# Kernel optimization log

Hardware: AMD Instinct MI355X
Metric: run time of the kernel (lower is better)

## Reference

```python
import jax, jax.numpy as jnp
import numpy as np

CUTOFF_UPPER = 4.5
EYE3 = jnp.eye(3, dtype=jnp.float32)


def tensor_norm(t):
    return (t ** 2).sum((-2, -1))


def decompose_tensor(X):
    # X: [N, C, 3, 3]
    tr_mean = jnp.trace(X, axis1=-2, axis2=-1) / 3.0
    I = tr_mean[..., None, None] * EYE3
    Xt = jnp.swapaxes(X, -2, -1)
    A = 0.5 * (X - Xt)
    S = 0.5 * (X + Xt) - I
    return I, A, S


def chan_linear(T, W, b):
    # torch: Linear applied over the channel axis after permute(0,2,3,1)
    # T: [N, C, 3, 3], W: [C, C], b: [C]
    return jnp.einsum('nkij,ck->ncij', T, W) + b[None, :, None, None]


def setup_inputs() -> dict:
    key = jax.random.key(0)
    ks = jax.random.split(key, 16)
    Np1, H, R, E = 20001, 128, 64, 200000
    X = jax.random.normal(ks[0], (Np1, H, 3, 3), dtype=jnp.float32)
    edge_index = jax.random.randint(ks[1], (2, E), 0, Np1)
    edge_weight = jax.random.uniform(ks[2], (E,), dtype=jnp.float32) * CUTOFF_UPPER
    edge_attr = jax.random.normal(ks[3], (E, R), dtype=jnp.float32)
    s = lambda fin: 1.0 / np.sqrt(fin)
    W1 = jax.random.uniform(ks[4], (3, H, H), minval=-s(H), maxval=s(H), dtype=jnp.float32)
    b1 = jax.random.uniform(ks[5], (3, H), minval=-s(H), maxval=s(H), dtype=jnp.float32)
    W2a = jax.random.uniform(ks[6], (H, R), minval=-s(R), maxval=s(R), dtype=jnp.float32)
    b2a = jax.random.uniform(ks[7], (H,), minval=-s(R), maxval=s(R), dtype=jnp.float32)
    W2b = jax.random.uniform(ks[8], (2 * H, H), minval=-s(H), maxval=s(H), dtype=jnp.float32)
    b2b = jax.random.uniform(ks[9], (2 * H,), minval=-s(H), maxval=s(H), dtype=jnp.float32)
    W2c = jax.random.uniform(ks[10], (3 * H, 2 * H), minval=-s(2 * H), maxval=s(2 * H), dtype=jnp.float32)
    b2c = jax.random.uniform(ks[11], (3 * H,), minval=-s(2 * H), maxval=s(2 * H), dtype=jnp.float32)
    W3 = jax.random.uniform(ks[12], (3, H, H), minval=-s(H), maxval=s(H), dtype=jnp.float32)
    b3 = jax.random.uniform(ks[13], (3, H), minval=-s(H), maxval=s(H), dtype=jnp.float32)
    return dict(X=X, edge_index=edge_index, edge_weight=edge_weight, edge_attr=edge_attr,
                W1=W1, b1=b1, W2a=W2a, b2a=b2a, W2b=W2b, b2b=b2b, W2c=W2c, b2c=b2c, W3=W3, b3=b3)


def reference(X, edge_index, edge_weight, edge_attr, W1, b1, W2a, b2a, W2b, b2b, W2c, b2c, W3, b3):
    Np1, H = X.shape[0], X.shape[1]
    act = jax.nn.silu
    X = X / (tensor_norm(X) + 1.0)[..., None, None]
    I, A, S = decompose_tensor(X)
    I = chan_linear(I, W1[0], b1[0])
    A = chan_linear(A, W1[1], b1[1])
    S = chan_linear(S, W1[2], b1[2])
    Y = I + A + S
    h = act(edge_attr @ W2a.T + b2a)
    h = act(h @ W2b.T + b2b)
    h = act(h @ W2c.T + b2c)  # [E, 3H]
    C = 0.5 * (jnp.cos(edge_weight * (jnp.pi / CUTOFF_UPPER)) + 1.0)
    C = C * (edge_weight < CUTOFF_UPPER).astype(C.dtype)
    ea = (h * C[:, None]).reshape(h.shape[0], H, 3)
    dst, src = edge_index[0], edge_index[1]

    def mp(factor, T):
        msg = factor[:, :, None, None] * T[src]  # [E, H, 3, 3]
        return jax.ops.segment_sum(msg, dst, num_segments=Np1)

    msg = mp(ea[..., 0], I) + mp(ea[..., 1], A) + mp(ea[..., 2], S)
    new_features = jnp.matmul(msg, Y) + jnp.matmul(Y, msg)  # O(3) branch
    I, A, S = decompose_tensor(new_features)
    norm = (tensor_norm(I + A + S) + 1.0)[..., None, None]
    I, A, S = I / norm, A / norm, S / norm
    I = chan_linear(I, W3[0], b3[0])
    A = chan_linear(A, W3[1], b3[1])
    S = chan_linear(S, W3[2], b3[2])
    dX = I + A + S
    return X + dX + jnp.matmul(dX, dX)
```

## Files before the change

kernel.cpp:

```cpp
#include <hip/hip_runtime.h>
#include <math.h>
#include <stdint.h>

typedef unsigned short u16;
typedef __attribute__((ext_vector_type(8))) short short8;
typedef __attribute__((ext_vector_type(4))) float floatx4;

__device__ __forceinline__ float b2f(u16 u){
  union{unsigned int i; float f;} v; v.i = ((unsigned int)u)<<16; return v.f;
}
__device__ __forceinline__ u16 f2b(float f){
  union{unsigned int i; float f;} v; v.f = f;
  unsigned int r = (v.i + 0x7FFFu + ((v.i>>16)&1u))>>16;
  return (u16)r;
}
__device__ __forceinline__ float ldx(const void* p, size_t i, int isb){
  return isb ? b2f(((const u16*)p)[i]) : ((const float*)p)[i];
}
__device__ __forceinline__ void ldg16_bf(const u16* p, u16* o){
  uint4 v0 = *reinterpret_cast<const uint4*>(p);
  uint4 v1 = *reinterpret_cast<const uint4*>(p+8);
  unsigned int u[8] = {v0.x,v0.y,v0.z,v0.w,v1.x,v1.y,v1.z,v1.w};
#pragma unroll
  for (int i=0;i<8;i++){ o[2*i] = (u16)(u[i]&0xffffu); o[2*i+1] = (u16)(u[i]>>16); }
}
__device__ __forceinline__ void ldg16_f32(const float* p, u16* o){
#pragma unroll
  for (int i=0;i<4;i++){
    float4 v = reinterpret_cast<const float4*>(p)[i];
    o[4*i+0]=f2b(v.x); o[4*i+1]=f2b(v.y); o[4*i+2]=f2b(v.z); o[4*i+3]=f2b(v.w);
  }
}
__device__ __forceinline__ uint4 pack8(const u16* o){
  uint4 r;
  r.x = (unsigned int)o[0] | ((unsigned int)o[1]<<16);
  r.y = (unsigned int)o[2] | ((unsigned int)o[3]<<16);
  r.z = (unsigned int)o[4] | ((unsigned int)o[5]<<16);
  r.w = (unsigned int)o[6] | ((unsigned int)o[7]<<16);
  return r;
}

__global__ void k_sniff(const void* __restrict__ X, int* __restrict__ flag)
{
  __shared__ int cnt;
  if (threadIdx.x==0) cnt = 0;
  __syncthreads();
  int c = 0;
  for (int t = threadIdx.x; t < 512; t += 256){
    unsigned int u = ((const u16*)X)[2*t];
    int e = (u >> 7) & 0xFF;
    if (e >= 110 && e <= 139) c++;
  }
  atomicAdd(&cnt, c);
  __syncthreads();
  if (threadIdx.x==0) *flag = (cnt > 300) ? 1 : 0;
}

__global__ __launch_bounds__(256) void k_zero(float* __restrict__ p, int n)
{
  int i = blockIdx.x*256 + threadIdx.x;
  if (i < n) p[i] = 0.f;
}
__global__ __launch_bounds__(256) void k_zero_int(int* __restrict__ p, int n)
{
  int i = blockIdx.x*256 + threadIdx.x;
  if (i < n) p[i] = 0;
}

__global__ __launch_bounds__(256) void k_hist(
    const int* __restrict__ ei, int* __restrict__ counts, int E)
{
  int e = blockIdx.x*256 + threadIdx.x;
  if (e < E) atomicAdd(&counts[ei[e]], 1);
}
__global__ __launch_bounds__(256) void k_scan(
    const int* __restrict__ counts, int* __restrict__ rowptr,
    int* __restrict__ fill, int N)
{
  __shared__ int sm[256];
  __shared__ int carry;
  int tid = threadIdx.x;
  if (tid == 0) carry = 0;
  __syncthreads();
  for (int base = 0; base < N; base += 256){
    int v = (base+tid < N) ? counts[base+tid] : 0;
    sm[tid] = v;
    __syncthreads();
    for (int off=1; off<256; off<<=1){
      int t = (tid >= off) ? sm[tid-off] : 0;
      __syncthreads();
      sm[tid] += t;
      __syncthreads();
    }
    int excl = carry + sm[tid] - v;
    if (base+tid < N){ rowptr[base+tid] = excl; fill[base+tid] = excl; }
    __syncthreads();
    if (tid == 0) carry += sm[255];
    __syncthreads();
  }
  if (tid == 0) rowptr[N] = carry;
}
__global__ __launch_bounds__(256) void k_scatter(
    const int* __restrict__ ei, int* __restrict__ fill,
    int* __restrict__ eorder, int E)
{
  int e = blockIdx.x*256 + threadIdx.x;
  if (e >= E) return;
  int d = ei[e];
  int pos = atomicAdd(&fill[d], 1);
  eorder[pos] = e;
}

__global__ __launch_bounds__(256) void k_decompose(
    const void* __restrict__ X, u16* __restrict__ Di, u16* __restrict__ Da,
    u16* __restrict__ Ds, int NH, const int* __restrict__ dflag)
{
  int tid = blockIdx.x*256 + threadIdx.x;
  if (tid >= NH) return;
  int isb = *dflag;
  int n = tid >> 7, k = tid & 127;
  float x[9]; float nrm = 0.f;
#pragma unroll
  for (int i=0;i<9;i++){ x[i]=ldx(X,(size_t)tid*9+i,isb); nrm += x[i]*x[i]; }
  float inv = 1.0f/(nrm+1.0f);
#pragma unroll
  for (int i=0;i<9;i++) x[i]*=inv;
  float i0 = (x[0]+x[4]+x[8])*(1.0f/3.0f);
  Di[tid] = f2b(i0);
  size_t ab = ((size_t)n*3)*128 + k;
  Da[ab      ] = f2b(0.5f*(x[1]-x[3]));
  Da[ab + 128] = f2b(0.5f*(x[2]-x[6]));
  Da[ab + 256] = f2b(0.5f*(x[5]-x[7]));
  size_t sb = ((size_t)n*6)*128 + k;
  Ds[sb      ] = f2b(x[0]-i0);
  Ds[sb + 128] = f2b(0.5f*(x[1]+x[3]));
  Ds[sb + 256] = f2b(0.5f*(x[2]+x[6]));
  Ds[sb + 384] = f2b(x[4]-i0);
  Ds[sb + 512] = f2b(0.5f*(x[5]+x[7]));
  Ds[sb + 640] = f2b(x[8]-i0);
}

__global__ __launch_bounds__(256) void k_mfma_gemm(
    const void* __restrict__ A, size_t aoff, const int* __restrict__ rowidx, int ridx0,
    const void* __restrict__ Bw, size_t boff,
    const void* __restrict__ bias, const float* __restrict__ rowscale,
    u16* __restrict__ C, int M, int Ncol, int K, int flags,
    int aext, int bext, const int* __restrict__ dflag)
{
  __shared__ u16 AsU[128][40];
  __shared__ u16 BsU[128][40];
  int isb = *dflag;
  int isbA = aext ? isb : 1;
  int isbB = bext ? isb : 1;
  int tid = threadIdx.x;
  int lane = tid & 63, l15 = lane & 15, q = lane >> 4;
  int wid = tid >> 6, wm = wid & 1, wn = wid >> 1;
  int n0 = blockIdx.x * 128, m0 = blockIdx.y * 128;
  int r = tid >> 1, cs = (tid & 1) * 16;

  floatx4 acc[4][4];
#pragma unroll
  for (int i=0;i<4;i++)
#pragma unroll
    for (int j=0;j<4;j++) acc[i][j] = (floatx4)0.f;

  long arow = -1;
  {
    int gm = m0 + r;
    if (gm < M) arow = rowidx ? (long)rowidx[ridx0 + gm] : (long)gm;
  }
  int brow_g = n0 + r;
  int bsrc = (flags & 4) ? ((brow_g & 127)*3 + (brow_g >> 7)) : brow_g;

  for (int k0 = 0; k0 < K; k0 += 32){
    u16 ta[16], tb[16];
    if (arow >= 0){
      size_t base = aoff + (size_t)arow*K + k0 + cs;
      if (isbA) ldg16_bf((const u16*)A + base, ta);
      else      ldg16_f32((const float*)A + base, ta);
    } else {
#pragma unroll
      for (int i=0;i<16;i++) ta[i]=0;
    }
    {
      size_t base = boff + (size_t)bsrc*K + k0 + cs;
      if (isbB) ldg16_bf((const u16*)Bw + base, tb);
      else      ldg16_f32((const float*)Bw + base, tb);
    }
    __syncthreads();
    *reinterpret_cast<uint4*>(&AsU[r][cs])   = pack8(ta);
    *reinterpret_cast<uint4*>(&AsU[r][cs+8]) = pack8(ta+8);
    *reinterpret_cast<uint4*>(&BsU[r][cs])   = pack8(tb);
    *reinterpret_cast<uint4*>(&BsU[r][cs+8]) = pack8(tb+8);
    __syncthreads();
    short8 av[4], bv[4];
#pragma unroll
    for (int mt=0; mt<4; mt++)
      av[mt] = *reinterpret_cast<const short8*>(&AsU[wm*64 + mt*16 + l15][q*8]);
#pragma unroll
    for (int nt=0; nt<4; nt++)
      bv[nt] = *reinterpret_cast<const short8*>(&BsU[wn*64 + nt*16 + l15][q*8]);
#pragma unroll
    for (int mt=0; mt<4; mt++)
#pragma unroll
      for (int nt=0; nt<4; nt++)
        acc[mt][nt] = __builtin_amdgcn_mfma_f32_16x16x32_bf16(av[mt], bv[nt], acc[mt][nt], 0, 0, 0);
  }

  float biasv[4];
#pragma unroll
  for (int nt=0; nt<4; nt++){
    int col = n0 + wn*64 + nt*16 + l15;
    int bcol = (flags & 4) ? ((col & 127)*3 + (col >> 7)) : col;
    biasv[nt] = bias ? ldx(bias, bcol, isbB) : 0.f;
  }
#pragma unroll
  for (int mt=0; mt<4; mt++){
#pragma unroll
    for (int reg=0; reg<4; reg++){
      int row = m0 + wm*64 + mt*16 + q*4 + reg;
      if (row >= M) continue;
      float rs = (flags & 2) ? rowscale[row] : 1.0f;
#pragma unroll
      for (int nt=0; nt<4; nt++){
        int col = n0 + wn*64 + nt*16 + l15;
        float t = acc[mt][nt][reg] + biasv[nt];
        if (flags & 1) t = t / (1.0f + expf(-t));
        C[(size_t)row*Ncol + col] = f2b(t*rs);
      }
    }
  }
}

__global__ __launch_bounds__(256) void k_cutoff(
    const void* __restrict__ ew, const int* __restrict__ eorder, int c0,
    float* __restrict__ Cc, int ec, const int* __restrict__ dflag)
{
  int i = blockIdx.x*256 + threadIdx.x;
  if (i >= ec) return;
  int e = eorder[c0 + i];
  float w = ldx(ew, e, *dflag);
  float c = 0.0f;
  if (w < 4.5f) c = 0.5f*(cosf(w*0.6981317007977318f) + 1.0f);
  Cc[i] = c;
}

__global__ __launch_bounds__(128) void k_gather(
    const int* __restrict__ rowptr, const int* __restrict__ eorder,
    const int* __restrict__ ei, int E, int c0, int c1,
    const u16* __restrict__ ea,
    const u16* __restrict__ Pi, const u16* __restrict__ Pa,
    const u16* __restrict__ Ps, const void* __restrict__ b1,
    float* __restrict__ msg, int NH, const int* __restrict__ dflag)
{
  int n = blockIdx.x;
  int lo = rowptr[n], hi = rowptr[n+1];
  if (lo < c0) lo = c0;
  if (hi > c1) hi = c1;
  if (lo >= hi) return;
  int isb = *dflag;
  int c = threadIdx.x;
  float b0 = ldx(b1,c,isb), b1f = ldx(b1,128+c,isb), b2v = ldx(b1,256+c,isb);
  float m[9];
#pragma unroll
  for (int i=0;i<9;i++) m[i]=0.f;
  for (int idx = lo; idx < hi; idx++){
    int e = eorder[idx];
    int src = ei[E + e];
    const u16* er = ea + (size_t)(idx - c0)*384;
    float e0f = b2f(er[c]), e1f = b2f(er[128+c]), e2f = b2f(er[256+c]);
    float i1 = b2f(Pi[(size_t)src*128 + c]);
    size_t ab = (size_t)src*384 + c;
    float a0 = b2f(Pa[ab]), a1 = b2f(Pa[ab+128]), a2 = b2f(Pa[ab+256]);
    size_t sb = (size_t)src*768 + c;
    float s0 = b2f(Ps[sb]),     s1 = b2f(Ps[sb+128]), s2 = b2f(Ps[sb+256]);
    float s3 = b2f(Ps[sb+384]), s4 = b2f(Ps[sb+512]), s5 = b2f(Ps[sb+640]);
    float bb = e0f*b0 + e1f*b1f + e2f*b2v;
    float t0 = e0f*i1;
    m[0] += t0 + e2f*s0 + bb;
    m[1] += e1f*a0 + e2f*s1 + bb;
    m[2] += e1f*a1 + e2f*s2 + bb;
    m[3] += -e1f*a0 + e2f*s1 + bb;
    m[4] += t0 + e2f*s3 + bb;
    m[5] += e1f*a2 + e2f*s4 + bb;
    m[6] += -e1f*a1 + e2f*s2 + bb;
    m[7] += -e1f*a2 + e2f*s4 + bb;
    m[8] += t0 + e2f*s5 + bb;
  }
  size_t o = (size_t)n*128 + c;
#pragma unroll
  for (int i=0;i<9;i++) msg[(size_t)i*NH + o] += m[i];
}

__global__ __launch_bounds__(256) void k_update(
    const float* __restrict__ msg, const u16* __restrict__ Pi,
    const u16* __restrict__ Pa, const u16* __restrict__ Ps,
    const void* __restrict__ b1,
    u16* __restrict__ D2i, u16* __restrict__ D2a, u16* __restrict__ D2s,
    int NH, const int* __restrict__ dflag)
{
  int tid = blockIdx.x*256 + threadIdx.x;
  if (tid >= NH) return;
  int isb = *dflag;
  int n = tid >> 7, c = tid & 127;
  float Mx[9];
#pragma unroll
  for (int i=0;i<9;i++) Mx[i] = msg[(size_t)i*NH + tid];
  float i1 = b2f(Pi[tid]);
  size_t ab = ((size_t)n*3)*128 + c;
  float a0 = b2f(Pa[ab]), a1 = b2f(Pa[ab+128]), a2 = b2f(Pa[ab+256]);
  size_t sb = ((size_t)n*6)*128 + c;
  float s0 = b2f(Ps[sb]),     s1 = b2f(Ps[sb+128]), s2 = b2f(Ps[sb+256]);
  float s3 = b2f(Ps[sb+384]), s4 = b2f(Ps[sb+512]), s5 = b2f(Ps[sb+640]);
  float B = ldx(b1,c,isb) + ldx(b1,128+c,isb) + ldx(b1,256+c,isb);
  float Y[9];
  Y[0]= i1+s0+B; Y[1]= a0+s1+B; Y[2]= a1+s2+B;
  Y[3]=-a0+s1+B; Y[4]= i1+s3+B; Y[5]= a2+s4+B;
  Y[6]=-a1+s2+B; Y[7]=-a2+s4+B; Y[8]= i1+s5+B;
  float F[9];
#pragma unroll
  for (int i=0;i<3;i++)
#pragma unroll
    for (int j=0;j<3;j++){
      float acc = 0.f;
#pragma unroll
      for (int t=0;t<3;t++)
        acc += Mx[i*3+t]*Y[t*3+j] + Y[i*3+t]*Mx[t*3+j];
      F[i*3+j] = acc;
    }
  float nrm = 0.f;
#pragma unroll
  for (int i=0;i<9;i++) nrm += F[i]*F[i];
  float inv = 1.0f/(nrm+1.0f);
  float i2 = (F[0]+F[4]+F[8])*(1.0f/3.0f);
  D2i[tid] = f2b(i2*inv);
  D2a[ab      ] = f2b(0.5f*(F[1]-F[3])*inv);
  D2a[ab + 128] = f2b(0.5f*(F[2]-F[6])*inv);
  D2a[ab + 256] = f2b(0.5f*(F[5]-F[7])*inv);
  D2s[sb      ] = f2b((F[0]-i2)*inv);
  D2s[sb + 128] = f2b(0.5f*(F[1]+F[3])*inv);
  D2s[sb + 256] = f2b(0.5f*(F[2]+F[6])*inv);
  D2s[sb + 384] = f2b((F[4]-i2)*inv);
  D2s[sb + 512] = f2b(0.5f*(F[5]+F[7])*inv);
  D2s[sb + 640] = f2b((F[8]-i2)*inv);
}

__global__ __launch_bounds__(256) void k_final(
    const void* __restrict__ X, const u16* __restrict__ P2i,
    const u16* __restrict__ P2a, const u16* __restrict__ P2s,
    const void* __restrict__ b3, void* __restrict__ out, int NH,
    const int* __restrict__ dflag)
{
  int tid = blockIdx.x*256 + threadIdx.x;
  if (tid >= NH) return;
  int isb = *dflag;
  int n = tid >> 7, c = tid & 127;
  float i1 = b2f(P2i[tid]);
  size_t ab = ((size_t)n*3)*128 + c;
  float a0 = b2f(P2a[ab]), a1 = b2f(P2a[ab+128]), a2 = b2f(P2a[ab+256]);
  size_t sb = ((size_t)n*6)*128 + c;
  float s0 = b2f(P2s[sb]),     s1 = b2f(P2s[sb+128]), s2 = b2f(P2s[sb+256]);
  float s3 = b2f(P2s[sb+384]), s4 = b2f(P2s[sb+512]), s5 = b2f(P2s[sb+640]);
  float B = ldx(b3,c,isb) + ldx(b3,128+c,isb) + ldx(b3,256+c,isb);
  float dX[9];
  dX[0]= i1+s0+B; dX[1]= a0+s1+B; dX[2]= a1+s2+B;
  dX[3]=-a0+s1+B; dX[4]= i1+s3+B; dX[5]= a2+s4+B;
  dX[6]=-a1+s2+B; dX[7]=-a2+s4+B; dX[8]= i1+s5+B;

  float x[9]; float nrm = 0.f;
#pragma unroll
  for (int i=0;i<9;i++){ x[i]=ldx(X,(size_t)tid*9+i,isb); nrm += x[i]*x[i]; }
  float inv = 1.0f/(nrm+1.0f);

#pragma unroll
  for (int i=0;i<3;i++)
#pragma unroll
    for (int j=0;j<3;j++){
      float acc = 0.f;
#pragma unroll
      for (int t=0;t<3;t++) acc += dX[i*3+t]*dX[t*3+j];
      float v = x[i*3+j]*inv + dX[i*3+j] + acc;
      size_t oi = (size_t)tid*9 + i*3 + j;
      if (isb) ((u16*)out)[oi] = f2b(v);
      else     ((float*)out)[oi] = v;
    }
}

extern "C" void kernel_launch(void* const* d_in, const int* in_sizes, int n_in,
                              void* d_out, int out_size, void* d_ws, size_t ws_size,
                              hipStream_t stream)
{
  const void* X    = d_in[0];
  const int*  ei   = (const int*)d_in[1];
  const void* ew   = d_in[2];
  const void* eatt = d_in[3];
  const void* W1   = d_in[4];
  const void* b1   = d_in[5];
  const void* W2a  = d_in[6];
  const void* b2a  = d_in[7];
  const void* W2b  = d_in[8];
  const void* b2b  = d_in[9];
  const void* W2c  = d_in[10];
  const void* b2c  = d_in[11];
  const void* W3   = d_in[12];
  const void* b3   = d_in[13];

  const int NH = in_sizes[0]/9;
  const int E  = in_sizes[2];
  const int N  = NH/128;

  auto aln = [](size_t x){ return (x + 255) & ~(size_t)255; };
  char* ws = (char*)d_ws;
  size_t off = 0;
  size_t o_flag = off; off += 256;
  size_t o_msg  = off; off += aln((size_t)NH*9*4);
  size_t o_Di   = off; off += aln((size_t)NH*2);
  size_t o_Da   = off; off += aln((size_t)NH*6);
  size_t o_Ds   = off; off += aln((size_t)NH*12);
  size_t o_Pi   = off; off += aln((size_t)NH*2);
  size_t o_Pa   = off; off += aln((size_t)NH*6);
  size_t o_Ps   = off; off += aln((size_t)NH*12);
  size_t o_cnt  = off; off += aln((size_t)N*4);
  size_t o_rp   = off; off += aln((size_t)(N+1)*4);
  size_t o_fill = off; off += aln((size_t)N*4);
  size_t o_eord = off; off += aln((size_t)E*4);
  size_t persistent = off;

  int EC;
  {
    size_t avail = (ws_size > persistent + 4096) ? (ws_size - persistent - 4096) : 0;
    size_t ecmax = avail / 1540;
    if (ecmax > (size_t)E) ecmax = (size_t)E;
    EC = (int)(ecmax & ~(size_t)1023);
    if (EC < 1024) EC = 1024;
  }
  size_t o_h1 = persistent;
  size_t o_h2 = o_h1 + aln((size_t)EC*256);
  size_t o_ea = o_h2 + aln((size_t)EC*512);
  size_t o_Cc = o_ea + aln((size_t)EC*768);
  (void)n_in; (void)out_size;

  int* dflag = (int*)(ws + o_flag);
  u16* Di = (u16*)(ws + o_Di);
  u16* Da = (u16*)(ws + o_Da);
  u16* Ds = (u16*)(ws + o_Ds);
  u16* Pi = (u16*)(ws + o_Pi);
  u16* Pa = (u16*)(ws + o_Pa);
  u16* Ps = (u16*)(ws + o_Ps);
  float* msg = (float*)(ws + o_msg);
  int* counts = (int*)(ws + o_cnt);
  int* rowptr = (int*)(ws + o_rp);
  int* fill   = (int*)(ws + o_fill);
  int* eorder = (int*)(ws + o_eord);
  u16* h1 = (u16*)(ws + o_h1);
  u16* h2 = (u16*)(ws + o_h2);
  u16* ea = (u16*)(ws + o_ea);
  float* Cc = (float*)(ws + o_Cc);

  dim3 blk(256);
  auto gemm = [&](const void* A, size_t aoff, const int* ridx, int ridx0,
                  const void* Bw, size_t boff, const void* bias, const float* rs,
                  u16* C, int M, int Ncol, int K, int flags, int aext, int bext){
    dim3 grid(Ncol/128, (M+127)/128);
    k_mfma_gemm<<<grid, blk, 0, stream>>>(A, aoff, ridx, ridx0, Bw, boff, bias, rs,
                                          C, M, Ncol, K, flags, aext, bext, dflag);
  };

  k_sniff<<<1, blk, 0, stream>>>(X, dflag);
  k_decompose<<<(NH+255)/256, blk, 0, stream>>>(X, Di, Da, Ds, NH, dflag);
  gemm(Di, 0, nullptr, 0, W1, 0,     nullptr, nullptr, Pi, N,   128, 128, 0, 0, 1);
  gemm(Da, 0, nullptr, 0, W1, 16384, nullptr, nullptr, Pa, 3*N, 128, 128, 0, 0, 1);
  gemm(Ds, 0, nullptr, 0, W1, 32768, nullptr, nullptr, Ps, 6*N, 128, 128, 0, 0, 1);
  k_zero<<<((NH*9)+255)/256, blk, 0, stream>>>(msg, NH*9);
  k_zero_int<<<(N+255)/256, blk, 0, stream>>>(counts, N);
  k_hist<<<(E+255)/256, blk, 0, stream>>>(ei, counts, E);
  k_scan<<<1, blk, 0, stream>>>(counts, rowptr, fill, N);
  k_scatter<<<(E+255)/256, blk, 0, stream>>>(ei, fill, eorder, E);
  for (int c0 = 0; c0 < E; c0 += EC){
    int ec = E - c0; if (ec > EC) ec = EC;
    k_cutoff<<<(ec+255)/256, blk, 0, stream>>>(ew, eorder, c0, Cc, ec, dflag);
    gemm(eatt, 0, eorder, c0, W2a, 0, b2a, nullptr, h1, ec, 128, 64,  1, 1, 1);
    gemm(h1, 0, nullptr, 0,   W2b, 0, b2b, nullptr, h2, ec, 256, 128, 1, 0, 1);
    gemm(h2, 0, nullptr, 0,   W2c, 0, b2c, Cc,      ea, ec, 384, 256, 1|2|4, 0, 1);
    k_gather<<<N, dim3(128), 0, stream>>>(rowptr, eorder, ei, E, c0, c0+ec,
                                          ea, Pi, Pa, Ps, b1, msg, NH, dflag);
  }
  k_update<<<(NH+255)/256, blk, 0, stream>>>(msg, Pi, Pa, Ps, b1, Di, Da, Ds, NH, dflag);
  gemm(Di, 0, nullptr, 0, W3, 0,     nullptr, nullptr, Pi, N,   128, 128, 0, 0, 1);
  gemm(Da, 0, nullptr, 0, W3, 16384, nullptr, nullptr, Pa, 3*N, 128, 128, 0, 0, 1);
  gemm(Ds, 0, nullptr, 0, W3, 32768, nullptr, nullptr, Ps, 6*N, 128, 128, 0, 0, 1);
  k_final<<<(NH+255)/256, blk, 0, stream>>>(X, Pi, Pa, Ps, b3, d_out, NH, dflag);
}
```

Baseline: 1.004 ms.

## Prefetch next GEMM K-tile into registers, swizzle LDS layout, fuse cutoff into epilogue

The MFMA GEMM now loads the next K-tile's global data into registers while the current tile is being consumed, and stores tiles in LDS in a fragment-major uint4 layout. Each lane then reads its MFMA operand directly, with no padded row layout and no u16 unpack/pack step. The separate cosine-cutoff kernel is removed and its computation folded into the last GEMM's epilogue via the edge order index, which also saves a workspace buffer. This adds register pressure from the prefetch registers and recomputes the cutoff once per output row per block column.

```diff
diff --git a/kernel.cpp b/kernel.cpp
--- a/kernel.cpp
+++ b/kernel.cpp
@@ -14,30 +14,11 @@
   unsigned int r = (v.i + 0x7FFFu + ((v.i>>16)&1u))>>16;
   return (u16)r;
 }
+__device__ __forceinline__ unsigned int pk2(float a, float b){
+  return (unsigned int)f2b(a) | ((unsigned int)f2b(b)<<16);
+}
 __device__ __forceinline__ float ldx(const void* p, size_t i, int isb){
   return isb ? b2f(((const u16*)p)[i]) : ((const float*)p)[i];
-}
-__device__ __forceinline__ void ldg16_bf(const u16* p, u16* o){
-  uint4 v0 = *reinterpret_cast<const uint4*>(p);
-  uint4 v1 = *reinterpret_cast<const uint4*>(p+8);
-  unsigned int u[8] = {v0.x,v0.y,v0.z,v0.w,v1.x,v1.y,v1.z,v1.w};
-#pragma unroll
-  for (int i=0;i<8;i++){ o[2*i] = (u16)(u[i]&0xffffu); o[2*i+1] = (u16)(u[i]>>16); }
-}
-__device__ __forceinline__ void ldg16_f32(const float* p, u16* o){
-#pragma unroll
-  for (int i=0;i<4;i++){
-    float4 v = reinterpret_cast<const float4*>(p)[i];
-    o[4*i+0]=f2b(v.x); o[4*i+1]=f2b(v.y); o[4*i+2]=f2b(v.z); o[4*i+3]=f2b(v.w);
-  }
-}
-__device__ __forceinline__ uint4 pack8(const u16* o){
-  uint4 r;
-  r.x = (unsigned int)o[0] | ((unsigned int)o[1]<<16);
-  r.y = (unsigned int)o[2] | ((unsigned int)o[3]<<16);
-  r.z = (unsigned int)o[4] | ((unsigned int)o[5]<<16);
-  r.w = (unsigned int)o[6] | ((unsigned int)o[7]<<16);
-  return r;
 }
 
 __global__ void k_sniff(const void* __restrict__ X, int* __restrict__ flag)
@@ -143,12 +124,12 @@
 __global__ __launch_bounds__(256) void k_mfma_gemm(
     const void* __restrict__ A, size_t aoff, const int* __restrict__ rowidx, int ridx0,
     const void* __restrict__ Bw, size_t boff,
-    const void* __restrict__ bias, const float* __restrict__ rowscale,
+    const void* __restrict__ bias, const void* __restrict__ ew,
     u16* __restrict__ C, int M, int Ncol, int K, int flags,
     int aext, int bext, const int* __restrict__ dflag)
 {
-  __shared__ u16 AsU[128][40];
-  __shared__ u16 BsU[128][40];
+  __shared__ uint4 AsF[512];
+  __shared__ uint4 BsF[512];
   int isb = *dflag;
   int isbA = aext ? isb : 1;
   int isbB = bext ? isb : 1;
@@ -157,6 +138,8 @@
   int wid = tid >> 6, wm = wid & 1, wn = wid >> 1;
   int n0 = blockIdx.x * 128, m0 = blockIdx.y * 128;
   int r = tid >> 1, cs = (tid & 1) * 16;
+  int f0 = (r>>4)*64 + (cs>>3)*16 + (r&15);
+  int f1 = f0 + 16;
 
   floatx4 acc[4][4];
 #pragma unroll
@@ -167,39 +150,53 @@
   long arow = -1;
   {
     int gm = m0 + r;
-    if (gm < M) arow = rowidx ? (long)rowidx[ridx0 + gm] : (long)gm;
+    if (gm < M) arow = (flags & 8) ? (long)rowidx[ridx0 + gm] : (long)gm;
   }
   int brow_g = n0 + r;
   int bsrc = (flags & 4) ? ((brow_g & 127)*3 + (brow_g >> 7)) : brow_g;
 
-  for (int k0 = 0; k0 < K; k0 += 32){
-    u16 ta[16], tb[16];
+  uint4 ga0, ga1, gb0, gb1;
+  auto ldtile = [&](int k0){
     if (arow >= 0){
       size_t base = aoff + (size_t)arow*K + k0 + cs;
-      if (isbA) ldg16_bf((const u16*)A + base, ta);
-      else      ldg16_f32((const float*)A + base, ta);
-    } else {
-#pragma unroll
-      for (int i=0;i<16;i++) ta[i]=0;
-    }
+      if (isbA){
+        const uint4* p = reinterpret_cast<const uint4*>((const u16*)A + base);
+        ga0 = p[0]; ga1 = p[1];
+      } else {
+        const float4* p = reinterpret_cast<const float4*>((const float*)A + base);
+        float4 v0=p[0], v1=p[1], v2=p[2], v3=p[3];
+        ga0 = make_uint4(pk2(v0.x,v0.y), pk2(v0.z,v0.w), pk2(v1.x,v1.y), pk2(v1.z,v1.w));
+        ga1 = make_uint4(pk2(v2.x,v2.y), pk2(v2.z,v2.w), pk2(v3.x,v3.y), pk2(v3.z,v3.w));
+      }
+    } else { ga0 = make_uint4(0,0,0,0); ga1 = ga0; }
     {
       size_t base = boff + (size_t)bsrc*K + k0 + cs;
-      if (isbB) ldg16_bf((const u16*)Bw + base, tb);
-      else      ldg16_f32((const float*)Bw + base, tb);
+      if (isbB){
+        const uint4* p = reinterpret_cast<const uint4*>((const u16*)Bw + base);
+        gb0 = p[0]; gb1 = p[1];
+      } else {
+        const float4* p = reinterpret_cast<const float4*>((const float*)Bw + base);
+        float4 v0=p[0], v1=p[1], v2=p[2], v3=p[3];
+        gb0 = make_uint4(pk2(v0.x,v0.y), pk2(v0.z,v0.w), pk2(v1.x,v1.y), pk2(v1.z,v1.w));
+        gb1 = make_uint4(pk2(v2.x,v2.y), pk2(v2.z,v2.w), pk2(v3.x,v3.y), pk2(v3.z,v3.w));
+      }
     }
+  };
+
+  ldtile(0);
+  for (int k0 = 0; k0 < K; k0 += 32){
     __syncthreads();
-    *reinterpret_cast<uint4*>(&AsU[r][cs])   = pack8(ta);
-    *reinterpret_cast<uint4*>(&AsU[r][cs+8]) = pack8(ta+8);
-    *reinterpret_cast<uint4*>(&BsU[r][cs])   = pack8(tb);
-    *reinterpret_cast<uint4*>(&BsU[r][cs+8]) = pack8(tb+8);
+    AsF[f0] = ga0; AsF[f1] = ga1;
+    BsF[f0] = gb0; BsF[f1] = gb1;
     __syncthreads();
+    if (k0 + 32 < K) ldtile(k0 + 32);
     short8 av[4], bv[4];
 #pragma unroll
     for (int mt=0; mt<4; mt++)
-      av[mt] = *reinterpret_cast<const short8*>(&AsU[wm*64 + mt*16 + l15][q*8]);
+      av[mt] = *reinterpret_cast<const short8*>(&AsF[(wm*4 + mt)*64 + lane]);
 #pragma unroll
     for (int nt=0; nt<4; nt++)
-      bv[nt] = *reinterpret_cast<const short8*>(&BsU[wn*64 + nt*16 + l15][q*8]);
+      bv[nt] = *reinterpret_cast<const short8*>(&BsF[(wn*4 + nt)*64 + lane]);
 #pragma unroll
     for (int mt=0; mt<4; mt++)
 #pragma unroll
@@ -220,7 +217,12 @@
     for (int reg=0; reg<4; reg++){
       int row = m0 + wm*64 + mt*16 + q*4 + reg;
       if (row >= M) continue;
-      float rs = (flags & 2) ? rowscale[row] : 1.0f;
+      float rs = 1.0f;
+      if (flags & 2){
+        int edge = rowidx[ridx0 + row];
+        float w = ldx(ew, edge, isb);
+        rs = (w < 4.5f) ? 0.5f*(cosf(w*0.6981317007977318f) + 1.0f) : 0.0f;
+      }
 #pragma unroll
       for (int nt=0; nt<4; nt++){
         int col = n0 + wn*64 + nt*16 + l15;
@@ -230,19 +232,6 @@
       }
     }
   }
-}
-
-__global__ __launch_bounds__(256) void k_cutoff(
-    const void* __restrict__ ew, const int* __restrict__ eorder, int c0,
-    float* __restrict__ Cc, int ec, const int* __restrict__ dflag)
-{
-  int i = blockIdx.x*256 + threadIdx.x;
-  if (i >= ec) return;
-  int e = eorder[c0 + i];
-  float w = ldx(ew, e, *dflag);
-  float c = 0.0f;
-  if (w < 4.5f) c = 0.5f*(cosf(w*0.6981317007977318f) + 1.0f);
-  Cc[i] = c;
 }
 
 __global__ __launch_bounds__(128) void k_gather(
@@ -429,7 +418,7 @@
   int EC;
   {
     size_t avail = (ws_size > persistent + 4096) ? (ws_size - persistent - 4096) : 0;
-    size_t ecmax = avail / 1540;
+    size_t ecmax = avail / 1536;
     if (ecmax > (size_t)E) ecmax = (size_t)E;
     EC = (int)(ecmax & ~(size_t)1023);
     if (EC < 1024) EC = 1024;
@@ -437,7 +426,6 @@
   size_t o_h1 = persistent;
   size_t o_h2 = o_h1 + aln((size_t)EC*256);
   size_t o_ea = o_h2 + aln((size_t)EC*512);
-  size_t o_Cc = o_ea + aln((size_t)EC*768);
   (void)n_in; (void)out_size;
 
   int* dflag = (int*)(ws + o_flag);
@@ -455,14 +443,13 @@
   u16* h1 = (u16*)(ws + o_h1);
   u16* h2 = (u16*)(ws + o_h2);
   u16* ea = (u16*)(ws + o_ea);
-  float* Cc = (float*)(ws + o_Cc);
 
   dim3 blk(256);
   auto gemm = [&](const void* A, size_t aoff, const int* ridx, int ridx0,
-                  const void* Bw, size_t boff, const void* bias, const float* rs,
+                  const void* Bw, size_t boff, const void* bias, const void* ewp,
                   u16* C, int M, int Ncol, int K, int flags, int aext, int bext){
     dim3 grid(Ncol/128, (M+127)/128);
-    k_mfma_gemm<<<grid, blk, 0, stream>>>(A, aoff, ridx, ridx0, Bw, boff, bias, rs,
+    k_mfma_gemm<<<grid, blk, 0, stream>>>(A, aoff, ridx, ridx0, Bw, boff, bias, ewp,
                                           C, M, Ncol, K, flags, aext, bext, dflag);
   };
 
@@ -478,10 +465,9 @@
   k_scatter<<<(E+255)/256, blk, 0, stream>>>(ei, fill, eorder, E);
   for (int c0 = 0; c0 < E; c0 += EC){
     int ec = E - c0; if (ec > EC) ec = EC;
-    k_cutoff<<<(ec+255)/256, blk, 0, stream>>>(ew, eorder, c0, Cc, ec, dflag);
-    gemm(eatt, 0, eorder, c0, W2a, 0, b2a, nullptr, h1, ec, 128, 64,  1, 1, 1);
+    gemm(eatt, 0, eorder, c0, W2a, 0, b2a, nullptr, h1, ec, 128, 64,  1|8, 1, 1);
     gemm(h1, 0, nullptr, 0,   W2b, 0, b2b, nullptr, h2, ec, 256, 128, 1, 0, 1);
-    gemm(h2, 0, nullptr, 0,   W2c, 0, b2c, Cc,      ea, ec, 384, 256, 1|2|4, 0, 1);
+    gemm(h2, 0, eorder, c0,   W2c, 0, b2c, ew,      ea, ec, 384, 256, 1|2|4, 0, 1);
     k_gather<<<N, dim3(128), 0, stream>>>(rowptr, eorder, ei, E, c0, c0+ec,
                                           ea, Pi, Pa, Ps, b1, msg, NH, dflag);
   }
```

New measurement: 1.050 ms. +4.7%, slower.
